# Performance work log

Hardware: AMD Instinct MI355X
Metric: run time of the kernel (lower is better)

Reference implementation:

```python
import jax, jax.numpy as jnp
import numpy as np

N_NODES = 50000
N_EDGES = 800000
IN_FEATS = 64
K = 4
OUT_FEATS = 256


def setup_inputs() -> dict:
    key = jax.random.key(0)
    k1, k2, k3, k4, k5 = jax.random.split(key, 5)
    signal = jax.random.normal(k1, (N_NODES, IN_FEATS), dtype=jnp.float32)
    src = jax.random.randint(k2, (N_EDGES,), 0, N_NODES, dtype=jnp.int32)
    dst = jax.random.randint(k3, (N_EDGES,), 0, N_NODES, dtype=jnp.int32)
    lambda_max = jnp.array([2.0], dtype=jnp.float32)  # normalized Laplacian bound
    W = jax.random.normal(k4, (IN_FEATS * K, OUT_FEATS), dtype=jnp.float32) * (1.0 / np.sqrt(IN_FEATS * K))
    b = jax.random.normal(k5, (OUT_FEATS,), dtype=jnp.float32) * 0.01
    return {"signal": signal, "src": src, "dst": dst, "lambda_max": lambda_max, "W": W, "b": b}


def reference(signal, src, dst, lambda_max, W, b):
    n = signal.shape[0]
    # in-degrees, clamped to >= 1, then D^{-1/2}
    deg = jax.ops.segment_sum(jnp.ones_like(dst, dtype=signal.dtype), dst, num_segments=n)
    d_sqrt = jnp.power(jnp.clip(deg, 1.0), -0.5)[:, None]  # [N,1]

    def unn_laplacian(x):
        # D^{-1/2} A D^{-1/2} x via gather-from-src, scatter-sum-to-dst
        h = (x * d_sqrt)[src]                                   # [E,f]
        agg = jax.ops.segment_sum(h, dst, num_segments=n)       # [N,f]
        return agg * d_sqrt

    X0 = signal
    Xs = [X0]
    if K > 1:
        re_norm = 2.0 / lambda_max  # broadcasts over nodes ([1] -> [N,f])
        X1 = -re_norm * unn_laplacian(X0) + X0 * (re_norm - 1.0)
        Xs.append(X1)
        for _ in range(2, K):
            Xi = -2.0 * re_norm * unn_laplacian(X1) + X1 * 2.0 * (re_norm - 1.0) - X0
            Xs.append(Xi)
            X1, X0 = Xi, X1
    Xt = jnp.concatenate(Xs, axis=1)  # [N, f*K]
    return jax.nn.relu(Xt @ W + b)
```

## Files before the change

### kernel.cpp

```cpp
#include <hip/hip_runtime.h>

#define NN 50000
#define NE 800000
#define F  64
#define OUTF 256
#define CAP 48
#define NT 3128

#define NPART 8
#define PART_NODES 6250
#define FILL_CHUNKS 256
#define CHUNK_E 3125

typedef __attribute__((ext_vector_type(8))) short    s16x8;
typedef __attribute__((ext_vector_type(8))) _Float16 f16x8;
typedef __attribute__((ext_vector_type(4))) float    f32x4;

static __device__ __forceinline__ unsigned short f2bf(float f) {
    unsigned u = __float_as_uint(f);
    u += 0x7fffu + ((u >> 16) & 1u);
    return (unsigned short)(u >> 16);
}
static __device__ __forceinline__ float bf2f(int h) {
    return __uint_as_float(((unsigned)(h & 0xffff)) << 16);
}
static __device__ __forceinline__ unsigned short f2h(float f) {
    _Float16 h = (_Float16)f;
    return __builtin_bit_cast(unsigned short, h);
}

__global__ __launch_bounds__(256) void fill_kernel(const int* __restrict__ src,
                                                   const int* __restrict__ dst,
                                                   int* __restrict__ cnt,
                                                   int* __restrict__ csr) {
    int part  = blockIdx.x & (NPART - 1);
    int chunk = blockIdx.x >> 3;
    int lo = part * PART_NODES;
    int e0 = chunk * CHUNK_E;
    int e1 = e0 + CHUNK_E;
    for (int e = e0 + threadIdx.x; e < e1; e += 256) {
        int d = dst[e];
        if ((unsigned)(d - lo) < (unsigned)PART_NODES) {
            int s = src[e];
            int k = atomicAdd(&cnt[d], 1);
            if (k < CAP) csr[d * CAP + k] = s;
        }
    }
}

__global__ void dsqrt_kernel(const int* __restrict__ cnt, float* __restrict__ dsq) {
    int n = blockIdx.x * blockDim.x + threadIdx.x;
    if (n < NN) dsq[n] = rsqrtf(fmaxf((float)cnt[n], 1.0f));
}


__global__ void copy0_kernel(const float* __restrict__ sig,
                             const float* __restrict__ dsq,
                             unsigned short* __restrict__ XrowH,
                             unsigned short* __restrict__ XrowL,
                             unsigned short* __restrict__ XfF) {
    int i = blockIdx.x * blockDim.x + threadIdx.x;
    if (i >= NN * 16) return;
    int n = i >> 4, fq = i & 15;
    float d = dsq[n];
    float4 v = *(const float4*)&sig[n * F + fq * 4];
    float yx = v.x * d, yy = v.y * d, yz = v.z * d, yw = v.w * d;
    unsigned short h0 = f2bf(yx), h1 = f2bf(yy), h2 = f2bf(yz), h3 = f2bf(yw);
    unsigned short l0 = f2bf(yx - bf2f(h0)), l1 = f2bf(yy - bf2f(h1));
    unsigned short l2 = f2bf(yz - bf2f(h2)), l3 = f2bf(yw - bf2f(h3));
    *(ushort4*)&XrowH[(size_t)n * 192 + fq * 4] = make_ushort4(h0, h1, h2, h3);
    *(ushort4*)&XrowL[(size_t)n * 192 + fq * 4] = make_ushort4(l0, l1, l2, l3);
    unsigned short u0 = f2h(v.x), u1 = f2h(v.y), u2 = f2h(v.z), u3 = f2h(v.w);
    int t = n >> 4, m = n & 15;
    int k0 = fq >> 3, qq = (fq >> 1) & 3, half = fq & 1;
    size_t base = ((size_t)((t * 8 + k0) * 64 + qq * 16 + m)) * 8 + half * 4;
    *(ushort4*)&XfF[base] = make_ushort4(u0, u1, u2, u3);
}

__global__ void convw_kernel(const float* __restrict__ W,
                             unsigned short* __restrict__ WfF) {
    int id = blockIdx.x * blockDim.x + threadIdx.x;
    if (id >= 8192) return;
    int lane = id & 63, k0 = (id >> 6) & 7, ct = id >> 9;
    int n = lane & 15, q = lane >> 4;
    s16x8 h;
    #pragma unroll
    for (int j = 0; j < 8; ++j) {
        float x = W[(k0 * 32 + q * 8 + j) * OUTF + ct * 16 + n];
        h[j] = (short)f2h(x);
    }
    ((s16x8*)WfF)[id] = h;
}

__global__ __launch_bounds__(256) void lap_kernel(const int* __restrict__ cnt,
                                                  const int* __restrict__ csr,
                                                  const float* __restrict__ dsq,
                                                  const float* __restrict__ lm,
                                                  unsigned short* __restrict__ XrowH,
                                                  unsigned short* __restrict__ XrowL,
                                                  unsigned short* __restrict__ XfF, int p) {
    int lane = threadIdx.x & 63;
    int half = lane >> 5;
    int sub  = lane & 31;
    int q2   = sub >> 4;
    int fq   = sub & 15;
    int wid  = (blockIdx.x * blockDim.x + threadIdx.x) >> 6;
    int n    = wid * 2 + half;
    if (n >= NN) return;
    int dgf = cnt[n];
    int dg  = min(dgf, CAP);
    int cin = p - 1;
    int foff = fq << 2;

    float ax = 0.f, ay = 0.f, az = 0.f, aw = 0.f;
    for (int k = 0; k < dg; k += 16) {
        int   s[8];
        float w[8];
        ushort4 h[8];
        #pragma unroll
        for (int j = 0; j < 8; ++j) {
            int slot = k + q2 + 2 * j;
            int ok   = slot < dg;
            int si   = csr[n * CAP + slot];
            s[j] = ok ? si : 0;
            w[j] = ok ? 1.0f : 0.0f;
        }
        #pragma unroll
        for (int j = 0; j < 8; ++j)
            h[j] = *(const ushort4*)&XrowH[((size_t)s[j] * 3 + cin) * 64 + foff];
        #pragma unroll
        for (int j = 0; j < 8; ++j) {
            ax += bf2f(h[j].x) * w[j];
            ay += bf2f(h[j].y) * w[j];
            az += bf2f(h[j].z) * w[j];
            aw += bf2f(h[j].w) * w[j];
        }
    }
    ax += __shfl_xor(ax, 16);
    ay += __shfl_xor(ay, 16);
    az += __shfl_xor(az, 16);
    aw += __shfl_xor(aw, 16);

    float rn = 2.0f / lm[0];
    float dn = dsq[n];
    float sq = sqrtf(fmaxf((float)dgf, 1.0f));
    ushort4 xh = *(const ushort4*)&XrowH[((size_t)n * 3 + cin) * 64 + foff];
    ushort4 xl = *(const ushort4*)&XrowL[((size_t)n * 3 + cin) * 64 + foff];
    float x1x = (bf2f(xh.x) + bf2f(xl.x)) * sq;
    float x1y = (bf2f(xh.y) + bf2f(xl.y)) * sq;
    float x1z = (bf2f(xh.z) + bf2f(xl.z)) * sq;
    float x1w = (bf2f(xh.w) + bf2f(xl.w)) * sq;
    float rx, ry, rz, rw;
    if (p == 1) {
        float c1 = rn - 1.0f;
        rx = -rn * dn * ax + x1x * c1;
        ry = -rn * dn * ay + x1y * c1;
        rz = -rn * dn * az + x1z * c1;
        rw = -rn * dn * aw + x1w * c1;
    } else {
        ushort4 zh = *(const ushort4*)&XrowH[((size_t)n * 3 + (p - 2)) * 64 + foff];
        ushort4 zl = *(const ushort4*)&XrowL[((size_t)n * 3 + (p - 2)) * 64 + foff];
        float c1 = 2.0f * (rn - 1.0f);
        rx = -2.0f * rn * dn * ax + x1x * c1 - (bf2f(zh.x) + bf2f(zl.x)) * sq;
        ry = -2.0f * rn * dn * ay + x1y * c1 - (bf2f(zh.y) + bf2f(zl.y)) * sq;
        rz = -2.0f * rn * dn * az + x1z * c1 - (bf2f(zh.z) + bf2f(zl.z)) * sq;
        rw = -2.0f * rn * dn * aw + x1w * c1 - (bf2f(zh.w) + bf2f(zl.w)) * sq;
    }

    float yx = rx * dn, yy = ry * dn, yz = rz * dn, yw = rw * dn;
    unsigned short yh0 = f2bf(yx), yh1 = f2bf(yy), yh2 = f2bf(yz), yh3 = f2bf(yw);
    if (q2 == 0) {
        if (p < 3)
            *(ushort4*)&XrowH[((size_t)n * 3 + p) * 64 + foff] = make_ushort4(yh0, yh1, yh2, yh3);
        unsigned short u0 = f2h(rx), u1 = f2h(ry), u2 = f2h(rz), u3 = f2h(rw);
        int t = n >> 4, m = n & 15;
        int k0 = p * 2 + (fq >> 3), qq = (fq >> 1) & 3, hf = fq & 1;
        size_t fbase = ((size_t)((t * 8 + k0) * 64 + qq * 16 + m)) * 8 + hf * 4;
        *(ushort4*)&XfF[fbase] = make_ushort4(u0, u1, u2, u3);
    } else if (p < 3) {
        unsigned short l0 = f2bf(yx - bf2f(yh0)), l1 = f2bf(yy - bf2f(yh1));
        unsigned short l2 = f2bf(yz - bf2f(yh2)), l3 = f2bf(yw - bf2f(yh3));
        *(ushort4*)&XrowL[((size_t)n * 3 + p) * 64 + foff] = make_ushort4(l0, l1, l2, l3);
    }
}

__global__ __launch_bounds__(512, 2) void gemm_kernel(const unsigned short* __restrict__ XfF,
                                                      const unsigned short* __restrict__ WfF,
                                                      const float* __restrict__ b,
                                                      float* __restrict__ out) {
    int lane = threadIdx.x & 63;
    int w    = threadIdx.x >> 6;
    int rh = w & 1, cg = w >> 1;
    int m = lane & 15, q = lane >> 4;
    int bt0 = blockIdx.x * 4;
    const f16x8* A = (const f16x8*)XfF;
    const f16x8* B = (const f16x8*)WfF;

    f32x4 acc[2][4];
    #pragma unroll
    for (int rt = 0; rt < 2; ++rt)
        #pragma unroll
        for (int c = 0; c < 4; ++c) acc[rt][c] = (f32x4){0.f, 0.f, 0.f, 0.f};

    #pragma unroll
    for (int k0 = 0; k0 < 8; ++k0) {
        f16x8 a[2];
        #pragma unroll
        for (int rt = 0; rt < 2; ++rt)
            a[rt] = A[((bt0 + rh * 2 + rt) * 8 + k0) * 64 + lane];
        #pragma unroll
        for (int c = 0; c < 4; ++c) {
            int ct = cg * 4 + c;
            f16x8 bh = B[(ct * 8 + k0) * 64 + lane];
            #pragma unroll
            for (int rt = 0; rt < 2; ++rt)
                acc[rt][c] = __builtin_amdgcn_mfma_f32_16x16x32_f16(a[rt], bh, acc[rt][c], 0, 0, 0);
        }
    }

    #pragma unroll
    for (int rt = 0; rt < 2; ++rt) {
        int rbase = (bt0 + rh * 2 + rt) * 16 + q * 4;
        #pragma unroll
        for (int c = 0; c < 4; ++c) {
            int col = (cg * 4 + c) * 16 + m;
            float bv = b[col];
            #pragma unroll
            for (int i = 0; i < 4; ++i) {
                int r = rbase + i;
                if (r < NN) out[r * OUTF + col] = fmaxf(acc[rt][c][i] + bv, 0.0f);
            }
        }
    }
}

extern "C" void kernel_launch(void* const* d_in, const int* in_sizes, int n_in,
                              void* d_out, int out_size, void* d_ws, size_t ws_size,
                              hipStream_t stream) {
    const float* signal     = (const float*)d_in[0];
    const int*   src        = (const int*)  d_in[1];
    const int*   dst        = (const int*)  d_in[2];
    const float* lambda_max = (const float*)d_in[3];
    const float* W          = (const float*)d_in[4];
    const float* b          = (const float*)d_in[5];
    float* out = (float*)d_out;

    int*   cnt = (int*)d_ws;
    int*   csr = cnt + NN;
    float* dsq = (float*)(csr + (size_t)NN * CAP);
    unsigned short* XrowH = (unsigned short*)(dsq + NN);
    unsigned short* XrowL = XrowH + (size_t)NN * 192;
    unsigned short* XfF   = XrowL + (size_t)NN * 192;
    unsigned short* WfF   = XfF + (size_t)NT * 4096;

    hipMemsetAsync(cnt, 0, NN * sizeof(int), stream);
    fill_kernel<<<NPART * FILL_CHUNKS, 256, 0, stream>>>(src, dst, cnt, csr);
    dsqrt_kernel<<<(NN + 255) / 256, 256, 0, stream>>>(cnt, dsq);
    copy0_kernel<<<(NN * 16 + 255) / 256, 256, 0, stream>>>(signal, dsq, XrowH, XrowL, XfF);
    convw_kernel<<<32, 256, 0, stream>>>(W, WfF);

    for (int p = 1; p <= 3; ++p)
        lap_kernel<<<NN / 8, 256, 0, stream>>>(cnt, csr, dsq, lambda_max, XrowH, XrowL, XfF, p);

    gemm_kernel<<<782, 512, 0, stream>>>(XfF, WfF, b, out);
}
```

Measured before the change: 220.3 us.

## Split Chebyshev feature rows into two 32-wide halves processed by separate block sweeps

The bf16 row buffers are split into two feature halves stored as separate planes, so each gathered row is 192 bytes per half instead of 384 interleaved. The lap kernel now assigns one node per wavefront, with 8 lanes per half-row and 8 neighbour groups, and uses block indexing to interleave the two half sweeps. The aim is a smaller gather working set per pass for better cache locality and more parallel neighbour loads. Non-temporal loads and stores are added for streaming data. In exchange, each neighbour index is read twice, the grid grows, and a three-step shuffle reduction is needed.

```diff
diff --git a/kernel.cpp b/kernel.cpp
--- a/kernel.cpp
+++ b/kernel.cpp
@@ -6,6 +6,7 @@
 #define OUTF 256
 #define CAP 48
 #define NT 3128
+#define HP (NN * 96)
 
 #define NPART 8
 #define PART_NODES 6250
@@ -15,6 +16,7 @@
 typedef __attribute__((ext_vector_type(8))) short    s16x8;
 typedef __attribute__((ext_vector_type(8))) _Float16 f16x8;
 typedef __attribute__((ext_vector_type(4))) float    f32x4;
+typedef __attribute__((ext_vector_type(4))) unsigned short u16x4;
 
 static __device__ __forceinline__ unsigned short f2bf(float f) {
     unsigned u = __float_as_uint(f);
@@ -68,8 +70,10 @@
     unsigned short h0 = f2bf(yx), h1 = f2bf(yy), h2 = f2bf(yz), h3 = f2bf(yw);
     unsigned short l0 = f2bf(yx - bf2f(h0)), l1 = f2bf(yy - bf2f(h1));
     unsigned short l2 = f2bf(yz - bf2f(h2)), l3 = f2bf(yw - bf2f(h3));
-    *(ushort4*)&XrowH[(size_t)n * 192 + fq * 4] = make_ushort4(h0, h1, h2, h3);
-    *(ushort4*)&XrowL[(size_t)n * 192 + fq * 4] = make_ushort4(l0, l1, l2, l3);
+    int sH = fq >> 3, fl = fq & 7;
+    size_t rbase = (size_t)sH * HP + (size_t)n * 96 + fl * 4;
+    *(u16x4*)&XrowH[rbase] = (u16x4){h0, h1, h2, h3};
+    *(u16x4*)&XrowL[rbase] = (u16x4){l0, l1, l2, l3};
     unsigned short u0 = f2h(v.x), u1 = f2h(v.y), u2 = f2h(v.z), u3 = f2h(v.w);
     int t = n >> 4, m = n & 15;
     int k0 = fq >> 3, qq = (fq >> 1) & 3, half = fq & 1;
@@ -99,88 +103,93 @@
                                                   unsigned short* __restrict__ XrowH,
                                                   unsigned short* __restrict__ XrowL,
                                                   unsigned short* __restrict__ XfF, int p) {
-    int lane = threadIdx.x & 63;
-    int half = lane >> 5;
-    int sub  = lane & 31;
-    int q2   = sub >> 4;
-    int fq   = sub & 15;
-    int wid  = (blockIdx.x * blockDim.x + threadIdx.x) >> 6;
-    int n    = wid * 2 + half;
-    if (n >= NN) return;
+    const int lane  = threadIdx.x & 63;
+    const int g     = lane >> 3;
+    const int fl    = lane & 7;
+    const int sweep = (blockIdx.x >> 2) & 1;
+    const int nb    = (blockIdx.x >> 3) * 4 + (blockIdx.x & 3);
+    const int n     = nb * 4 + (threadIdx.x >> 6);
+    const int cin   = p - 1;
+
+    unsigned short* Xh = XrowH + (size_t)sweep * HP;
+    unsigned short* Xl = XrowL + (size_t)sweep * HP;
+
     int dgf = cnt[n];
     int dg  = min(dgf, CAP);
-    int cin = p - 1;
-    int foff = fq << 2;
-
-    float ax = 0.f, ay = 0.f, az = 0.f, aw = 0.f;
-    for (int k = 0; k < dg; k += 16) {
-        int   s[8];
-        float w[8];
-        ushort4 h[8];
-        #pragma unroll
-        for (int j = 0; j < 8; ++j) {
-            int slot = k + q2 + 2 * j;
+
+    float a0 = 0.f, a1 = 0.f, a2 = 0.f, a3 = 0.f;
+    for (int k = 0; k < dg; k += 32) {
+        int sj[4]; float wj[4];
+        #pragma unroll
+        for (int j = 0; j < 4; ++j) {
+            int slot = k + g + 8 * j;
             int ok   = slot < dg;
-            int si   = csr[n * CAP + slot];
-            s[j] = ok ? si : 0;
-            w[j] = ok ? 1.0f : 0.0f;
-        }
-        #pragma unroll
-        for (int j = 0; j < 8; ++j)
-            h[j] = *(const ushort4*)&XrowH[((size_t)s[j] * 3 + cin) * 64 + foff];
-        #pragma unroll
-        for (int j = 0; j < 8; ++j) {
-            ax += bf2f(h[j].x) * w[j];
-            ay += bf2f(h[j].y) * w[j];
-            az += bf2f(h[j].z) * w[j];
-            aw += bf2f(h[j].w) * w[j];
-        }
-    }
-    ax += __shfl_xor(ax, 16);
-    ay += __shfl_xor(ay, 16);
-    az += __shfl_xor(az, 16);
-    aw += __shfl_xor(aw, 16);
-
-    float rn = 2.0f / lm[0];
-    float dn = dsq[n];
-    float sq = sqrtf(fmaxf((float)dgf, 1.0f));
-    ushort4 xh = *(const ushort4*)&XrowH[((size_t)n * 3 + cin) * 64 + foff];
-    ushort4 xl = *(const ushort4*)&XrowL[((size_t)n * 3 + cin) * 64 + foff];
-    float x1x = (bf2f(xh.x) + bf2f(xl.x)) * sq;
-    float x1y = (bf2f(xh.y) + bf2f(xl.y)) * sq;
-    float x1z = (bf2f(xh.z) + bf2f(xl.z)) * sq;
-    float x1w = (bf2f(xh.w) + bf2f(xl.w)) * sq;
-    float rx, ry, rz, rw;
+            int si   = __builtin_nontemporal_load(&csr[n * CAP + slot]);
+            sj[j] = ok ? si : 0;
+            wj[j] = ok ? 1.f : 0.f;
+        }
+        u16x4 hj[4];
+        #pragma unroll
+        for (int j = 0; j < 4; ++j)
+            hj[j] = *(const u16x4*)&Xh[(size_t)sj[j] * 96 + cin * 32 + fl * 4];
+        #pragma unroll
+        for (int j = 0; j < 4; ++j) {
+            a0 += bf2f(hj[j][0]) * wj[j];
+            a1 += bf2f(hj[j][1]) * wj[j];
+            a2 += bf2f(hj[j][2]) * wj[j];
+            a3 += bf2f(hj[j][3]) * wj[j];
+        }
+    }
+    a0 += __shfl_xor(a0, 8); a0 += __shfl_xor(a0, 16); a0 += __shfl_xor(a0, 32);
+    a1 += __shfl_xor(a1, 8); a1 += __shfl_xor(a1, 16); a1 += __shfl_xor(a1, 32);
+    a2 += __shfl_xor(a2, 8); a2 += __shfl_xor(a2, 16); a2 += __shfl_xor(a2, 32);
+    a3 += __shfl_xor(a3, 8); a3 += __shfl_xor(a3, 16); a3 += __shfl_xor(a3, 32);
+
+    const float rn = 2.0f / lm[0];
+    const float dn = dsq[n];
+    const float sq = sqrtf(fmaxf((float)dgf, 1.0f));
+    const size_t ro = (size_t)n * 96 + cin * 32 + fl * 4;
+    u16x4 xh = *(const u16x4*)&Xh[ro];
+    u16x4 xl = __builtin_nontemporal_load((const u16x4*)&Xl[ro]);
+    float x10 = (bf2f(xh[0]) + bf2f(xl[0])) * sq;
+    float x11 = (bf2f(xh[1]) + bf2f(xl[1])) * sq;
+    float x12 = (bf2f(xh[2]) + bf2f(xl[2])) * sq;
+    float x13 = (bf2f(xh[3]) + bf2f(xl[3])) * sq;
+    float r0, r1, r2, r3;
     if (p == 1) {
         float c1 = rn - 1.0f;
-        rx = -rn * dn * ax + x1x * c1;
-        ry = -rn * dn * ay + x1y * c1;
-        rz = -rn * dn * az + x1z * c1;
-        rw = -rn * dn * aw + x1w * c1;
+        r0 = -rn * dn * a0 + x10 * c1;
+        r1 = -rn * dn * a1 + x11 * c1;
+        r2 = -rn * dn * a2 + x12 * c1;
+        r3 = -rn * dn * a3 + x13 * c1;
     } else {
-        ushort4 zh = *(const ushort4*)&XrowH[((size_t)n * 3 + (p - 2)) * 64 + foff];
-        ushort4 zl = *(const ushort4*)&XrowL[((size_t)n * 3 + (p - 2)) * 64 + foff];
+        const size_t zo = (size_t)n * 96 + (p - 2) * 32 + fl * 4;
+        u16x4 zh = __builtin_nontemporal_load((const u16x4*)&Xh[zo]);
+        u16x4 zl = __builtin_nontemporal_load((const u16x4*)&Xl[zo]);
         float c1 = 2.0f * (rn - 1.0f);
-        rx = -2.0f * rn * dn * ax + x1x * c1 - (bf2f(zh.x) + bf2f(zl.x)) * sq;
-        ry = -2.0f * rn * dn * ay + x1y * c1 - (bf2f(zh.y) + bf2f(zl.y)) * sq;
-        rz = -2.0f * rn * dn * az + x1z * c1 - (bf2f(zh.z) + bf2f(zl.z)) * sq;
-        rw = -2.0f * rn * dn * aw + x1w * c1 - (bf2f(zh.w) + bf2f(zl.w)) * sq;
-    }
-
-    float yx = rx * dn, yy = ry * dn, yz = rz * dn, yw = rw * dn;
-    unsigned short yh0 = f2bf(yx), yh1 = f2bf(yy), yh2 = f2bf(yz), yh3 = f2bf(yw);
-    if (q2 == 0) {
-        if (p < 3)
-            *(ushort4*)&XrowH[((size_t)n * 3 + p) * 64 + foff] = make_ushort4(yh0, yh1, yh2, yh3);
-        unsigned short u0 = f2h(rx), u1 = f2h(ry), u2 = f2h(rz), u3 = f2h(rw);
+        r0 = -2.f * rn * dn * a0 + x10 * c1 - (bf2f(zh[0]) + bf2f(zl[0])) * sq;
+        r1 = -2.f * rn * dn * a1 + x11 * c1 - (bf2f(zh[1]) + bf2f(zl[1])) * sq;
+        r2 = -2.f * rn * dn * a2 + x12 * c1 - (bf2f(zh[2]) + bf2f(zl[2])) * sq;
+        r3 = -2.f * rn * dn * a3 + x13 * c1 - (bf2f(zh[3]) + bf2f(zl[3])) * sq;
+    }
+
+    float y0 = r0 * dn, y1 = r1 * dn, y2 = r2 * dn, y3 = r3 * dn;
+    unsigned short yh0 = f2bf(y0), yh1 = f2bf(y1), yh2 = f2bf(y2), yh3 = f2bf(y3);
+    if (g == 0) {
+        if (p < 3) {
+            u16x4 v = {yh0, yh1, yh2, yh3};
+            __builtin_nontemporal_store(v, (u16x4*)&Xh[(size_t)n * 96 + p * 32 + fl * 4]);
+        }
+    } else if (g == 1 && p < 3) {
+        u16x4 v = {f2bf(y0 - bf2f(yh0)), f2bf(y1 - bf2f(yh1)),
+                   f2bf(y2 - bf2f(yh2)), f2bf(y3 - bf2f(yh3))};
+        __builtin_nontemporal_store(v, (u16x4*)&Xl[(size_t)n * 96 + p * 32 + fl * 4]);
+    } else if (g == 2) {
         int t = n >> 4, m = n & 15;
-        int k0 = p * 2 + (fq >> 3), qq = (fq >> 1) & 3, hf = fq & 1;
+        int k0 = p * 2 + sweep, qq = (fl >> 1) & 3, hf = fl & 1;
         size_t fbase = ((size_t)((t * 8 + k0) * 64 + qq * 16 + m)) * 8 + hf * 4;
-        *(ushort4*)&XfF[fbase] = make_ushort4(u0, u1, u2, u3);
-    } else if (p < 3) {
-        unsigned short l0 = f2bf(yx - bf2f(yh0)), l1 = f2bf(yy - bf2f(yh1));
-        unsigned short l2 = f2bf(yz - bf2f(yh2)), l3 = f2bf(yw - bf2f(yh3));
-        *(ushort4*)&XrowL[((size_t)n * 3 + p) * 64 + foff] = make_ushort4(l0, l1, l2, l3);
+        u16x4 v = {f2h(r0), f2h(r1), f2h(r2), f2h(r3)};
+        __builtin_nontemporal_store(v, (u16x4*)&XfF[fbase]);
     }
 }
 
@@ -247,10 +256,10 @@
 
     int*   cnt = (int*)d_ws;
     int*   csr = cnt + NN;
-    float* dsq = (float*)(csr + (size_t)NN * CAP);
+    float* dsq = (float*)(csr + (size_t)NN * CAP + 64);
     unsigned short* XrowH = (unsigned short*)(dsq + NN);
-    unsigned short* XrowL = XrowH + (size_t)NN * 192;
-    unsigned short* XfF   = XrowL + (size_t)NN * 192;
+    unsigned short* XrowL = XrowH + (size_t)2 * HP;
+    unsigned short* XfF   = XrowL + (size_t)2 * HP;
     unsigned short* WfF   = XfF + (size_t)NT * 4096;
 
     hipMemsetAsync(cnt, 0, NN * sizeof(int), stream);
@@ -260,7 +269,7 @@
     convw_kernel<<<32, 256, 0, stream>>>(W, WfF);
 
     for (int p = 1; p <= 3; ++p)
-        lap_kernel<<<NN / 8, 256, 0, stream>>>(cnt, csr, dsq, lambda_max, XrowH, XrowL, XfF, p);
+        lap_kernel<<<25000, 256, 0, stream>>>(cnt, csr, dsq, lambda_max, XrowH, XrowL, XfF, p);
 
     gemm_kernel<<<782, 512, 0, stream>>>(XfF, WfF, b, out);
 }
```

Measured after the change: 310.5 us. 41.0% more time.

## Assign one wavefront per node in Laplacian gather with unrolled neighbor loads

Applied to the files above, without the earlier changes.

The Laplacian kernel now maps a whole 64-lane wavefront to each node instead of half a wavefront. The four lane quarters split the neighbor slots, and a reduction across the quarters combines the partial sums. The first 32 neighbor slots are gathered in one fully unrolled batch, and a short tail handles slots beyond 32, which replaces the variable-trip loop. Different quarters now handle the three output stores, and the grid is doubled. This is meant to expose more memory-level parallelism per node and spread the writes, at the cost of twice as many wavefronts and some wasted loads on padded slots for low-degree nodes.

```diff
diff --git a/kernel.cpp b/kernel.cpp
--- a/kernel.cpp
+++ b/kernel.cpp
@@ -99,47 +99,55 @@
                                                   unsigned short* __restrict__ XrowH,
                                                   unsigned short* __restrict__ XrowL,
                                                   unsigned short* __restrict__ XfF, int p) {
-    int lane = threadIdx.x & 63;
-    int half = lane >> 5;
-    int sub  = lane & 31;
-    int q2   = sub >> 4;
-    int fq   = sub & 15;
-    int wid  = (blockIdx.x * blockDim.x + threadIdx.x) >> 6;
-    int n    = wid * 2 + half;
-    if (n >= NN) return;
+    const int lane = threadIdx.x & 63;
+    const int q    = lane >> 4;
+    const int fq   = lane & 15;
+    const int n    = (blockIdx.x * blockDim.x + threadIdx.x) >> 6;
+    const int cin  = p - 1;
+    const int foff = fq << 2;
     int dgf = cnt[n];
     int dg  = min(dgf, CAP);
-    int cin = p - 1;
-    int foff = fq << 2;
-
+
+    int   s[8]; float w[8];
+    #pragma unroll
+    for (int j = 0; j < 8; ++j) {
+        int slot = q + 4 * j;
+        int ok   = slot < dg;
+        int si   = csr[n * CAP + slot];
+        s[j] = ok ? si : n;
+        w[j] = ok ? 1.0f : 0.0f;
+    }
+    ushort4 h[8];
+    #pragma unroll
+    for (int j = 0; j < 8; ++j)
+        h[j] = *(const ushort4*)&XrowH[((size_t)s[j] * 3 + cin) * 64 + foff];
     float ax = 0.f, ay = 0.f, az = 0.f, aw = 0.f;
-    for (int k = 0; k < dg; k += 16) {
-        int   s[8];
-        float w[8];
-        ushort4 h[8];
-        #pragma unroll
-        for (int j = 0; j < 8; ++j) {
-            int slot = k + q2 + 2 * j;
+    #pragma unroll
+    for (int j = 0; j < 8; ++j) {
+        ax += bf2f(h[j].x) * w[j];
+        ay += bf2f(h[j].y) * w[j];
+        az += bf2f(h[j].z) * w[j];
+        aw += bf2f(h[j].w) * w[j];
+    }
+    if (dg > 32) {
+        #pragma unroll
+        for (int j = 8; j < 12; ++j) {
+            int slot = q + 4 * j;
             int ok   = slot < dg;
             int si   = csr[n * CAP + slot];
-            s[j] = ok ? si : 0;
-            w[j] = ok ? 1.0f : 0.0f;
-        }
-        #pragma unroll
-        for (int j = 0; j < 8; ++j)
-            h[j] = *(const ushort4*)&XrowH[((size_t)s[j] * 3 + cin) * 64 + foff];
-        #pragma unroll
-        for (int j = 0; j < 8; ++j) {
-            ax += bf2f(h[j].x) * w[j];
-            ay += bf2f(h[j].y) * w[j];
-            az += bf2f(h[j].z) * w[j];
-            aw += bf2f(h[j].w) * w[j];
-        }
-    }
-    ax += __shfl_xor(ax, 16);
-    ay += __shfl_xor(ay, 16);
-    az += __shfl_xor(az, 16);
-    aw += __shfl_xor(aw, 16);
+            int sj   = ok ? si : n;
+            float wj = ok ? 1.0f : 0.0f;
+            ushort4 hh = *(const ushort4*)&XrowH[((size_t)sj * 3 + cin) * 64 + foff];
+            ax += bf2f(hh.x) * wj;
+            ay += bf2f(hh.y) * wj;
+            az += bf2f(hh.z) * wj;
+            aw += bf2f(hh.w) * wj;
+        }
+    }
+    ax += __shfl_xor(ax, 16); ax += __shfl_xor(ax, 32);
+    ay += __shfl_xor(ay, 16); ay += __shfl_xor(ay, 32);
+    az += __shfl_xor(az, 16); az += __shfl_xor(az, 32);
+    aw += __shfl_xor(aw, 16); aw += __shfl_xor(aw, 32);
 
     float rn = 2.0f / lm[0];
     float dn = dsq[n];
@@ -169,18 +177,18 @@
 
     float yx = rx * dn, yy = ry * dn, yz = rz * dn, yw = rw * dn;
     unsigned short yh0 = f2bf(yx), yh1 = f2bf(yy), yh2 = f2bf(yz), yh3 = f2bf(yw);
-    if (q2 == 0) {
-        if (p < 3)
-            *(ushort4*)&XrowH[((size_t)n * 3 + p) * 64 + foff] = make_ushort4(yh0, yh1, yh2, yh3);
+    if (q == 0 && p < 3) {
+        *(ushort4*)&XrowH[((size_t)n * 3 + p) * 64 + foff] = make_ushort4(yh0, yh1, yh2, yh3);
+    } else if (q == 2 && p < 3) {
+        unsigned short l0 = f2bf(yx - bf2f(yh0)), l1 = f2bf(yy - bf2f(yh1));
+        unsigned short l2 = f2bf(yz - bf2f(yh2)), l3 = f2bf(yw - bf2f(yh3));
+        *(ushort4*)&XrowL[((size_t)n * 3 + p) * 64 + foff] = make_ushort4(l0, l1, l2, l3);
+    } else if (q == 1) {
         unsigned short u0 = f2h(rx), u1 = f2h(ry), u2 = f2h(rz), u3 = f2h(rw);
         int t = n >> 4, m = n & 15;
         int k0 = p * 2 + (fq >> 3), qq = (fq >> 1) & 3, hf = fq & 1;
         size_t fbase = ((size_t)((t * 8 + k0) * 64 + qq * 16 + m)) * 8 + hf * 4;
         *(ushort4*)&XfF[fbase] = make_ushort4(u0, u1, u2, u3);
-    } else if (p < 3) {
-        unsigned short l0 = f2bf(yx - bf2f(yh0)), l1 = f2bf(yy - bf2f(yh1));
-        unsigned short l2 = f2bf(yz - bf2f(yh2)), l3 = f2bf(yw - bf2f(yh3));
-        *(ushort4*)&XrowL[((size_t)n * 3 + p) * 64 + foff] = make_ushort4(l0, l1, l2, l3);
     }
 }
 
@@ -260,7 +268,7 @@
     convw_kernel<<<32, 256, 0, stream>>>(W, WfF);
 
     for (int p = 1; p <= 3; ++p)
-        lap_kernel<<<NN / 8, 256, 0, stream>>>(cnt, csr, dsq, lambda_max, XrowH, XrowL, XfF, p);
+        lap_kernel<<<NN / 4, 256, 0, stream>>>(cnt, csr, dsq, lambda_max, XrowH, XrowL, XfF, p);
 
     gemm_kernel<<<782, 512, 0, stream>>>(XfF, WfF, b, out);
 }
```

Result: slower. 233.8 us (+6.2%).
